# Kernel optimization log

Measured on AMD Instinct MI355X. Metric: run time of the kernel, lower is better.

The kernel has to match this reference:

```python
import jax, jax.numpy as jnp
import numpy as np

B, D, L, N = 16, 256, 4096, 4096
MAX_SPAN = 64


def setup_inputs() -> dict:
    key = jax.random.key(0)
    k1, k2, k3 = jax.random.split(key, 3)
    features = jax.random.normal(k1, (B, D, L), dtype=jnp.float32)
    # TOI spans: start in [0, L - MAX_SPAN), length in [1, MAX_SPAN]
    start = jax.random.randint(k2, (B, N), 0, L - MAX_SPAN, dtype=jnp.int32)
    length = jax.random.randint(k3, (B, N), 1, MAX_SPAN + 1, dtype=jnp.int32)
    tois = jnp.stack([start, start + length], axis=-1)  # [B, N, 2]
    return {"features": features, "tois": tois}


def _pool_one(feat, toi):
    # feat: [D, L], toi: [N, 2] -> [N, 3*D]
    start = toi[:, 0]
    end = toi[:, 1]
    # cumsum with zero-padding column: [D, L+1]
    cs = jnp.concatenate(
        [jnp.zeros((feat.shape[0], 1), dtype=feat.dtype), jnp.cumsum(feat, axis=1)],
        axis=1,
    )
    span_len = (end - start).astype(feat.dtype)
    avg = (cs[:, end] - cs[:, start]) / span_len          # [D, N]
    head = feat[:, start]                                  # [D, N]
    tail = feat[:, end - 1]                                # [D, N]
    return jnp.concatenate([head, avg, tail], axis=0).T    # [N, 3*D]


def reference(features, tois):
    # features: [B, D, L] float32, tois: [B, N, 2] int32
    pooled = jax.vmap(_pool_one)(features, tois)           # [B, N, 3*D]
    out = pooled.reshape(-1, pooled.shape[-1])             # [B*N, 3*D]
    n = tois.shape[1]
    counts = jnp.cumsum(jnp.full((tois.shape[0],), n, dtype=jnp.int32))
    return out, counts
```

## Files before the change

kernel.cpp:

```cpp
#include <hip/hip_runtime.h>
#include <hip/hip_bf16.h>

constexpr int B = 16;
constexpr int D = 256;
constexpr int L = 4096;
constexpr int N = 4096;
constexpr int TS = 64;
constexpr int NT = L / TS;

typedef float v4f __attribute__((ext_vector_type(4)));

__global__ __launch_bounds__(256) void row_scan(const float* __restrict__ feat,
                                                float* __restrict__ P,
                                                float* __restrict__ cs_t) {
    __shared__ float tsum[NT];
    int row = blockIdx.x;
    int tid = threadIdx.x;
    const float4* fr = (const float4*)(feat + (size_t)row * L);

    float s[4];
    #pragma unroll
    for (int r = 0; r < 4; ++r) {
        float4 v = fr[r * 256 + tid];
        s[r] = (v.x + v.y) + (v.z + v.w);
    }
    #pragma unroll
    for (int r = 0; r < 4; ++r) {
        float v = s[r];
        #pragma unroll
        for (int off = 1; off < 16; off <<= 1) v += __shfl_xor(v, off, 64);
        if ((tid & 15) == 0) tsum[r * 16 + (tid >> 4)] = v;
    }
    __syncthreads();

    if (tid < NT) {
        float v = tsum[tid];
        float incl = v;
        #pragma unroll
        for (int off = 1; off < 64; off <<= 1) {
            float u = __shfl_up(incl, off, 64);
            if (tid >= off) incl += u;
        }
        P[row * NT + tid] = incl - v;
        if (tid == NT - 1) {
            int b = row >> 8, d = row & 255;
            cs_t[((size_t)b * (L + 1) + L) * D + d] = incl;
        }
    }
}

__global__ __launch_bounds__(256) void transpose_scan(const float* __restrict__ feat,
                                                      const float* __restrict__ P,
                                                      float* __restrict__ cs_t) {
    __shared__ float tile[64][65];
    __shared__ float poff[64];
    int bid = blockIdx.x;
    int t   = bid & 63;
    int dt  = (bid >> 6) & 3;
    int b   = bid >> 8;
    int tid = threadIdx.x;
    int ll  = tid & 63;
    int k0  = tid >> 6;
    int d0  = dt * 64;
    int l0  = t * TS;

    if (tid < 64) poff[tid] = P[(b * D + d0 + tid) * NT + t];
    #pragma unroll
    for (int k = 0; k < 16; ++k) {
        int dd = k0 + k * 4;
        tile[dd][ll] = feat[((size_t)(b * D + d0 + dd)) * L + l0 + ll];
    }
    __syncthreads();

    #pragma unroll
    for (int r = 0; r < 16; ++r) {
        int dd = k0 * 16 + r;
        float v = tile[dd][ll];
        float incl = v;
        #pragma unroll
        for (int off = 1; off < 64; off <<= 1) {
            float u = __shfl_up(incl, off, 64);
            if (ll >= off) incl += u;
        }
        tile[dd][ll] = (incl - v) + poff[dd];
    }
    __syncthreads();

    #pragma unroll
    for (int k = 0; k < 16; ++k) {
        int l = k0 + k * 4;
        cs_t[((size_t)b * (L + 1) + l0 + l) * D + d0 + ll] = tile[ll][l];
    }
}

__global__ __launch_bounds__(256) void pool_queries(const float* __restrict__ cs_t,
                                                    const int* __restrict__ tois,
                                                    float* __restrict__ out) {
    int gw   = (blockIdx.x * blockDim.x + threadIdx.x) >> 6;
    int lane = threadIdx.x & 63;
    int b = gw >> 12;
    int2 se = ((const int2*)tois)[gw];
    int s = se.x, e = se.y;

    const size_t base = (size_t)b * (L + 1);
    const v4f* r_s = (const v4f*)(cs_t + (base + s) * D);
    const v4f* r_e = (const v4f*)(cs_t + (base + e) * D);

    v4f cs0 = r_s[lane];
    v4f cs1 = r_s[lane + 64];
    v4f ce1 = r_e[lane - 64];
    v4f ce0 = r_e[lane];

    float inv = 1.0f / (float)(e - s);
    v4f head = cs1 - cs0;
    v4f avg  = (ce0 - cs0) * inv;
    v4f tail = ce0 - ce1;

    v4f* orow = (v4f*)(out + (size_t)gw * (3 * D));
    __builtin_nontemporal_store(head, orow + lane);
    __builtin_nontemporal_store(avg,  orow + 64 + lane);
    __builtin_nontemporal_store(tail, orow + 128 + lane);

    if (gw == 0 && lane < B)
        out[(size_t)B * N * (3 * D) + lane] = (float)((lane + 1) * N);
}

__global__ __launch_bounds__(256) void pool_direct(const float* __restrict__ feat,
                                                   const int* __restrict__ tois,
                                                   float* __restrict__ out) {
    int gw   = (blockIdx.x * blockDim.x + threadIdx.x) >> 6;
    int lane = threadIdx.x & 63;
    if (gw >= B * N) return;
    int b = gw >> 12;
    int s = tois[gw * 2 + 0];
    int e = tois[gw * 2 + 1];
    float inv = 1.0f / (float)(e - s);
    float* orow = out + (size_t)gw * (3 * D);
    #pragma unroll
    for (int c = 0; c < 4; ++c) {
        int d = c * 64 + lane;
        const float* f = feat + ((size_t)(b * D + d)) * L;
        float sum = 0.f;
        for (int j = s; j < e; ++j) sum += f[j];
        orow[d]         = f[s];
        orow[D + d]     = sum * inv;
        orow[2 * D + d] = f[e - 1];
    }
    if (gw == 0 && lane < B)
        out[(size_t)B * N * (3 * D) + lane] = (float)((lane + 1) * N);
}

extern "C" void kernel_launch(void* const* d_in, const int* in_sizes, int n_in,
                              void* d_out, int out_size, void* d_ws, size_t ws_size,
                              hipStream_t stream) {
    const float* feat = (const float*)d_in[0];
    const int*   tois = (const int*)d_in[1];
    float*       out  = (float*)d_out;

    const size_t cs_elems = (size_t)B * (L + 1) * D;
    const size_t p_elems  = (size_t)B * D * NT;
    const size_t need     = (cs_elems + p_elems) * sizeof(float);

    if (ws_size >= need) {
        float* cs_t = (float*)d_ws;
        float* P    = cs_t + cs_elems;

        row_scan<<<B * D, 256, 0, stream>>>(feat, P, cs_t);
        transpose_scan<<<B * (D / 64) * NT, 256, 0, stream>>>(feat, P, cs_t);
        pool_queries<<<B * N / 4, 256, 0, stream>>>(cs_t, tois, out);
    } else {
        pool_direct<<<B * N / 4, 256, 0, stream>>>(feat, tois, out);
    }
}
```

Before: 293.1 us.

## Vectorize transpose_scan loads/stores and remap pool_queries block order across XCDs

transpose_scan now loads float4 per thread and does a 4-element serial prefix followed by a 16-lane shuffle scan, instead of a 64-lane shuffle scan per element. This removes one sync and one shared-memory round trip, and the final stores become float4. pool_queries remaps block IDs so that consecutive query chunks go to the same XCD (bid&7 striding), which is meant to improve L2 locality for cs_t rows of the same batch. The float4 stores read four different tile rows, which may cause some bank conflicts.

```diff
diff --git a/kernel.cpp b/kernel.cpp
--- a/kernel.cpp
+++ b/kernel.cpp
@@ -59,45 +59,58 @@
     int dt  = (bid >> 6) & 3;
     int b   = bid >> 8;
     int tid = threadIdx.x;
-    int ll  = tid & 63;
-    int k0  = tid >> 6;
+    int lane = tid & 63;
+    int w    = tid >> 6;
+    int q    = lane >> 4;
+    int p    = lane & 15;
     int d0  = dt * 64;
     int l0  = t * TS;
 
     if (tid < 64) poff[tid] = P[(b * D + d0 + tid) * NT + t];
+    __syncthreads();
+
+    const float* fbase = feat + (size_t)(b * D + d0) * L + l0;
     #pragma unroll
-    for (int k = 0; k < 16; ++k) {
-        int dd = k0 + k * 4;
-        tile[dd][ll] = feat[((size_t)(b * D + d0 + dd)) * L + l0 + ll];
+    for (int r = 0; r < 4; ++r) {
+        int dd = w * 16 + r * 4 + q;
+        v4f v = *(const v4f*)(fbase + (size_t)dd * L + p * 4);
+        float x = v.x, y = v.y, z = v.z, u = v.w;
+        float tot = ((x + y) + z) + u;
+        float incl = tot;
+        #pragma unroll
+        for (int off = 1; off < 16; off <<= 1) {
+            float s = __shfl_up(incl, off, 16);
+            if (p >= off) incl += s;
+        }
+        float base = (incl - tot) + poff[dd];
+        tile[dd][p * 4 + 0] = base;
+        tile[dd][p * 4 + 1] = base + x;
+        tile[dd][p * 4 + 2] = base + (x + y);
+        tile[dd][p * 4 + 3] = base + ((x + y) + z);
     }
     __syncthreads();
 
     #pragma unroll
-    for (int r = 0; r < 16; ++r) {
-        int dd = k0 * 16 + r;
-        float v = tile[dd][ll];
-        float incl = v;
-        #pragma unroll
-        for (int off = 1; off < 64; off <<= 1) {
-            float u = __shfl_up(incl, off, 64);
-            if (ll >= off) incl += u;
-        }
-        tile[dd][ll] = (incl - v) + poff[dd];
-    }
-    __syncthreads();
-
-    #pragma unroll
-    for (int k = 0; k < 16; ++k) {
-        int l = k0 + k * 4;
-        cs_t[((size_t)b * (L + 1) + l0 + l) * D + d0 + ll] = tile[ll][l];
+    for (int k = 0; k < 4; ++k) {
+        int l  = k * 16 + (tid >> 4);
+        int d4 = (tid & 15) * 4;
+        v4f val;
+        val.x = tile[d4 + 0][l];
+        val.y = tile[d4 + 1][l];
+        val.z = tile[d4 + 2][l];
+        val.w = tile[d4 + 3][l];
+        *(v4f*)(cs_t + ((size_t)b * (L + 1) + l0 + l) * D + d0 + d4) = val;
     }
 }
 
 __global__ __launch_bounds__(256) void pool_queries(const float* __restrict__ cs_t,
                                                     const int* __restrict__ tois,
                                                     float* __restrict__ out) {
-    int gw   = (blockIdx.x * blockDim.x + threadIdx.x) >> 6;
-    int lane = threadIdx.x & 63;
+    int nchunk = (int)gridDim.x >> 3;
+    int bid    = blockIdx.x;
+    int nbid   = (bid & 7) * nchunk + (bid >> 3);
+    int gw     = nbid * 4 + (threadIdx.x >> 6);
+    int lane   = threadIdx.x & 63;
     int b = gw >> 12;
     int2 se = ((const int2*)tois)[gw];
     int s = se.x, e = se.y;
```

Result: faster. 271.7 us (-7.3%).

## Bin queries by start tile and pool from local shared-memory prefix windows

Applied to the files above, without the earlier changes.

Replaces the global cumulative-sum table (full scan, transpose, and a large cs_t write and read back) with a counting sort of queries by start tile, followed by a pool kernel. Each pool block loads a 128-wide window of features into shared memory, builds a local prefix sum, and answers the queries binned to that tile. Because every span is at most 64 long and starts inside the tile, the local window covers it. This removes the multi-megabyte intermediate buffer traffic. In exchange it adds several small launches (memset, histogram, offsets, scatter) plus atomics, and load balance now depends on how many queries land in each bin.

```diff
diff --git a/kernel.cpp b/kernel.cpp
--- a/kernel.cpp
+++ b/kernel.cpp
@@ -1,128 +1,149 @@
 #include <hip/hip_runtime.h>
-#include <hip/hip_bf16.h>
 
 constexpr int B = 16;
 constexpr int D = 256;
 constexpr int L = 4096;
 constexpr int N = 4096;
 constexpr int TS = 64;
-constexpr int NT = L / TS;
+constexpr int NTL = L / TS;
+constexpr int NBIN = B * NTL;
+constexpr int WIN = 128;
+constexpr int SD = 65;
 
 typedef float v4f __attribute__((ext_vector_type(4)));
 
-__global__ __launch_bounds__(256) void row_scan(const float* __restrict__ feat,
-                                                float* __restrict__ P,
-                                                float* __restrict__ cs_t) {
-    __shared__ float tsum[NT];
-    int row = blockIdx.x;
+
+__global__ __launch_bounds__(256) void q_hist(const int* __restrict__ tois,
+                                              int* __restrict__ cnt) {
+    __shared__ int h[NTL];
     int tid = threadIdx.x;
-    const float4* fr = (const float4*)(feat + (size_t)row * L);
+    if (tid < NTL) h[tid] = 0;
+    __syncthreads();
+    int q = blockIdx.x * 256 + tid;
+    int s = tois[q * 2];
+    atomicAdd(&h[s >> 6], 1);
+    __syncthreads();
+    int b = blockIdx.x >> 4;
+    if (tid < NTL) { int v = h[tid]; if (v) atomicAdd(&cnt[b * NTL + tid], v); }
+}
 
-    float s[4];
+__global__ __launch_bounds__(1024) void q_offsets(const int* __restrict__ cnt,
+                                                  int* __restrict__ off) {
+    __shared__ int wt[16];
+    int tid = threadIdx.x;
+    int v = cnt[tid];
+    int incl = v;
     #pragma unroll
-    for (int r = 0; r < 4; ++r) {
-        float4 v = fr[r * 256 + tid];
-        s[r] = (v.x + v.y) + (v.z + v.w);
+    for (int o = 1; o < 64; o <<= 1) {
+        int u = __shfl_up(incl, o, 64);
+        if ((tid & 63) >= o) incl += u;
     }
+    if ((tid & 63) == 63) wt[tid >> 6] = incl;
+    __syncthreads();
+    if (tid == 0) {
+        int a = 0;
+        #pragma unroll
+        for (int i = 0; i < 16; ++i) { int t2 = wt[i]; wt[i] = a; a += t2; }
+        off[NBIN] = a;
+    }
+    __syncthreads();
+    off[tid] = wt[tid >> 6] + incl - v;
+}
+
+__global__ __launch_bounds__(256) void q_scatter(const int* __restrict__ tois,
+                                                 const int* __restrict__ off,
+                                                 int* __restrict__ cur,
+                                                 int* __restrict__ qlist,
+                                                 float* __restrict__ out) {
+    int tid = threadIdx.x;
+    int q = blockIdx.x * 256 + tid;
+    int s = tois[q * 2];
+    int b = q >> 12;
+    int bin = b * NTL + (s >> 6);
+    int pos = atomicAdd(&cur[bin], 1);
+    qlist[off[bin] + pos] = q;
+    if (q < B) out[(size_t)B * N * (3 * D) + q] = (float)((q + 1) * N);
+}
+
+__global__ __launch_bounds__(256, 4) void pool(const float* __restrict__ feat,
+                                               const int* __restrict__ tois,
+                                               const int* __restrict__ off,
+                                               const int* __restrict__ qlist,
+                                               float* __restrict__ out) {
+    __shared__ float cs[WIN][SD];
+    __shared__ float qtot[4][64];
+    __shared__ float qoff[4][64];
+
+    int bid  = blockIdx.x;
+    int nbid = (bid & 7) * ((int)gridDim.x >> 3) + (bid >> 3);
+    int dq = nbid & 3;
+    int t  = (nbid >> 2) & 63;
+    int b  = nbid >> 8;
+    int bin = b * NTL + t;
+    int qs0 = off[bin];
+    int nq  = off[bin + 1] - qs0;
+    if (nq == 0) return;
+
+    int tid = threadIdx.x, lane = tid & 63, wv = tid >> 6;
+    int d0 = dq * 64, l0 = t * TS;
+
+    const float* fb = feat + ((size_t)(b * D + d0)) * L + l0;
     #pragma unroll
-    for (int r = 0; r < 4; ++r) {
-        float v = s[r];
-        #pragma unroll
-        for (int off = 1; off < 16; off <<= 1) v += __shfl_xor(v, off, 64);
-        if ((tid & 15) == 0) tsum[r * 16 + (tid >> 4)] = v;
+    for (int k = 0; k < 8; ++k) {
+        int g = k * 256 + tid;
+        int r = g >> 5, cc = g & 31;
+        v4f v = *(const v4f*)(fb + (size_t)r * L + cc * 4);
+        cs[cc * 4 + 0][r] = v.x;
+        cs[cc * 4 + 1][r] = v.y;
+        cs[cc * 4 + 2][r] = v.z;
+        cs[cc * 4 + 3][r] = v.w;
     }
     __syncthreads();
 
-    if (tid < NT) {
-        float v = tsum[tid];
-        float incl = v;
+    {
+        float c = 0.f;
         #pragma unroll
-        for (int off = 1; off < 64; off <<= 1) {
-            float u = __shfl_up(incl, off, 64);
-            if (tid >= off) incl += u;
+        for (int i = 0; i < 32; ++i) {
+            int l = wv * 32 + i;
+            float v = cs[l][lane];
+            cs[l][lane] = c;
+            c += v;
         }
-        P[row * NT + tid] = incl - v;
-        if (tid == NT - 1) {
-            int b = row >> 8, d = row & 255;
-            cs_t[((size_t)b * (L + 1) + L) * D + d] = incl;
-        }
+        qtot[wv][lane] = c;
     }
-}
-
-__global__ __launch_bounds__(256) void transpose_scan(const float* __restrict__ feat,
-                                                      const float* __restrict__ P,
-                                                      float* __restrict__ cs_t) {
-    __shared__ float tile[64][65];
-    __shared__ float poff[64];
-    int bid = blockIdx.x;
-    int t   = bid & 63;
-    int dt  = (bid >> 6) & 3;
-    int b   = bid >> 8;
-    int tid = threadIdx.x;
-    int ll  = tid & 63;
-    int k0  = tid >> 6;
-    int d0  = dt * 64;
-    int l0  = t * TS;
-
-    if (tid < 64) poff[tid] = P[(b * D + d0 + tid) * NT + t];
-    #pragma unroll
-    for (int k = 0; k < 16; ++k) {
-        int dd = k0 + k * 4;
-        tile[dd][ll] = feat[((size_t)(b * D + d0 + dd)) * L + l0 + ll];
+    __syncthreads();
+    if (tid < 64) {
+        float o = 0.f;
+        #pragma unroll
+        for (int qr = 0; qr < 4; ++qr) { float v = qtot[qr][tid]; qoff[qr][tid] = o; o += v; }
+    }
+    __syncthreads();
+    if (wv) {
+        float o = qoff[wv][lane];
+        #pragma unroll
+        for (int i = 0; i < 32; ++i) cs[wv * 32 + i][lane] += o;
     }
     __syncthreads();
 
-    #pragma unroll
-    for (int r = 0; r < 16; ++r) {
-        int dd = k0 * 16 + r;
-        float v = tile[dd][ll];
-        float incl = v;
-        #pragma unroll
-        for (int off = 1; off < 64; off <<= 1) {
-            float u = __shfl_up(incl, off, 64);
-            if (ll >= off) incl += u;
-        }
-        tile[dd][ll] = (incl - v) + poff[dd];
+    const int2* tp = (const int2*)tois;
+    for (int it = wv; it < nq; it += 4) {
+        int q = qlist[qs0 + it];
+        int2 se = tp[q];
+        int si = se.x - l0;
+        int ei = se.y - l0;
+        float a0 = cs[si][lane];
+        float a1 = cs[si + 1][lane];
+        float e0 = cs[ei][lane];
+        float e1 = cs[ei - 1][lane];
+        float inv = 1.0f / (float)(se.y - se.x);
+        float head = a1 - a0;
+        float avg  = (e0 - a0) * inv;
+        float tail = e0 - e1;
+        float* orow = out + (size_t)q * (3 * D) + d0 + lane;
+        __builtin_nontemporal_store(head, orow);
+        __builtin_nontemporal_store(avg,  orow + D);
+        __builtin_nontemporal_store(tail, orow + 2 * D);
     }
-    __syncthreads();
-
-    #pragma unroll
-    for (int k = 0; k < 16; ++k) {
-        int l = k0 + k * 4;
-        cs_t[((size_t)b * (L + 1) + l0 + l) * D + d0 + ll] = tile[ll][l];
-    }
-}
-
-__global__ __launch_bounds__(256) void pool_queries(const float* __restrict__ cs_t,
-                                                    const int* __restrict__ tois,
-                                                    float* __restrict__ out) {
-    int gw   = (blockIdx.x * blockDim.x + threadIdx.x) >> 6;
-    int lane = threadIdx.x & 63;
-    int b = gw >> 12;
-    int2 se = ((const int2*)tois)[gw];
-    int s = se.x, e = se.y;
-
-    const size_t base = (size_t)b * (L + 1);
-    const v4f* r_s = (const v4f*)(cs_t + (base + s) * D);
-    const v4f* r_e = (const v4f*)(cs_t + (base + e) * D);
-
-    v4f cs0 = r_s[lane];
-    v4f cs1 = r_s[lane + 64];
-    v4f ce1 = r_e[lane - 64];
-    v4f ce0 = r_e[lane];
-
-    float inv = 1.0f / (float)(e - s);
-    v4f head = cs1 - cs0;
-    v4f avg  = (ce0 - cs0) * inv;
-    v4f tail = ce0 - ce1;
-
-    v4f* orow = (v4f*)(out + (size_t)gw * (3 * D));
-    __builtin_nontemporal_store(head, orow + lane);
-    __builtin_nontemporal_store(avg,  orow + 64 + lane);
-    __builtin_nontemporal_store(tail, orow + 128 + lane);
-
-    if (gw == 0 && lane < B)
-        out[(size_t)B * N * (3 * D) + lane] = (float)((lane + 1) * N);
 }
 
 __global__ __launch_bounds__(256) void pool_direct(const float* __restrict__ feat,
@@ -157,17 +178,18 @@
     const int*   tois = (const int*)d_in[1];
     float*       out  = (float*)d_out;
 
-    const size_t cs_elems = (size_t)B * (L + 1) * D;
-    const size_t p_elems  = (size_t)B * D * NT;
-    const size_t need     = (cs_elems + p_elems) * sizeof(float);
+    int* cnt   = (int*)d_ws;
+    int* cur   = cnt + NBIN;
+    int* off   = cur + NBIN;
+    int* qlist = off + NBIN + 1;
+    const size_t need = (size_t)(NBIN * 2 + NBIN + 1 + B * N) * sizeof(int);
 
     if (ws_size >= need) {
-        float* cs_t = (float*)d_ws;
-        float* P    = cs_t + cs_elems;
-
-        row_scan<<<B * D, 256, 0, stream>>>(feat, P, cs_t);
-        transpose_scan<<<B * (D / 64) * NT, 256, 0, stream>>>(feat, P, cs_t);
-        pool_queries<<<B * N / 4, 256, 0, stream>>>(cs_t, tois, out);
+        hipMemsetAsync(cnt, 0, (size_t)NBIN * 2 * sizeof(int), stream);
+        q_hist   <<<B * N / 256, 256, 0, stream>>>(tois, cnt);
+        q_offsets<<<1, 1024, 0, stream>>>(cnt, off);
+        q_scatter<<<B * N / 256, 256, 0, stream>>>(tois, off, cur, qlist, out);
+        pool     <<<B * (D / 64) * NTL, 256, 0, stream>>>(feat, tois, off, qlist, out);
     } else {
         pool_direct<<<B * N / 4, 256, 0, stream>>>(feat, tois, out);
     }
```

Measured after the change: 270.0 us. 7.9% less time.
